# Kernel tuning notes

Measured on AMD Instinct MI355X. Metric: run time of the kernel, lower is better.

## Reference

```python
import jax, jax.numpy as jnp
import numpy as np

N_NODES = 50000
N_EDGES = 1000000
IN_CH = 256
HID_CH = 128
HEADS = 2
OUT_CH = 3
NEG_SLOPE = 0.2  # PyG GATConv default leaky_relu slope


def setup_inputs() -> dict:
    key = jax.random.key(0)
    ks = jax.random.split(key, 10)
    s = 0.1
    x = jax.random.normal(ks[0], (N_NODES, IN_CH), dtype=jnp.float32)
    edge_index = jax.random.randint(ks[1], (2, N_EDGES), 0, N_NODES, dtype=jnp.int64)
    # GATConv layer 1 (heads=2, concat=True)
    W1 = jax.random.normal(ks[2], (IN_CH, HEADS * HID_CH), dtype=jnp.float32) * s
    a_src1 = jax.random.normal(ks[3], (HEADS, HID_CH), dtype=jnp.float32) * s
    a_dst1 = jax.random.normal(ks[4], (HEADS, HID_CH), dtype=jnp.float32) * s
    b1 = jnp.zeros((HEADS * HID_CH,), dtype=jnp.float32)
    # GATConv layer 2 (heads=1, concat=False)
    W2 = jax.random.normal(ks[5], (HEADS * HID_CH, OUT_CH), dtype=jnp.float32) * s
    a_src2 = jax.random.normal(ks[6], (1, OUT_CH), dtype=jnp.float32) * s
    a_dst2 = jax.random.normal(ks[7], (1, OUT_CH), dtype=jnp.float32) * s
    b2 = jnp.zeros((OUT_CH,), dtype=jnp.float32)
    return dict(x=x, edge_index=edge_index, W1=W1, a_src1=a_src1, a_dst1=a_dst1,
                b1=b1, W2=W2, a_src2=a_src2, a_dst2=a_dst2, b2=b2)


def gat_layer(x, edge_index, W, a_src, a_dst, b, concat):
    # x: [N, F_in]; W: [F_in, H*C]; a_src/a_dst: [H, C]
    n = x.shape[0]
    H, C = a_src.shape
    h = (x @ W).reshape(n, H, C)                       # [N, H, C]
    al_s = jnp.einsum('nhc,hc->nh', h, a_src)          # [N, H]
    al_d = jnp.einsum('nhc,hc->nh', h, a_dst)          # [N, H]
    src, dst = edge_index[0], edge_index[1]
    e = jax.nn.leaky_relu(al_s[src] + al_d[dst], NEG_SLOPE)   # [E, H]
    # segment softmax over incoming edges of each dst node
    e_max = jax.ops.segment_max(e, dst, num_segments=n)       # [N, H]
    w = jnp.exp(e - e_max[dst])                                # [E, H]
    denom = jax.ops.segment_sum(w, dst, num_segments=n)        # [N, H]
    alpha = w / jnp.maximum(denom[dst], 1e-16)                 # [E, H]
    out = jax.ops.segment_sum(h[src] * alpha[:, :, None], dst, num_segments=n)  # [N, H, C]
    out = out.reshape(n, H * C) if concat else out.mean(axis=1)
    return out + b


def reference(x, edge_index, W1, a_src1, a_dst1, b1, W2, a_src2, a_dst2, b2):
    # dropout(p=0.6) is identity in eval mode
    h = jax.nn.elu(gat_layer(x, edge_index, W1, a_src1, a_dst1, b1, concat=True))
    h = gat_layer(h, edge_index, W2, a_src2, a_dst2, b2, concat=False)
    return jax.nn.log_softmax(h, axis=1)
```

## Files before the change

kernel.cpp:

```cpp
#include <hip/hip_runtime.h>

#define N_NODES 50000
#define N_EDGES 1000000
#define FIN 256
#define F1  256
#define OUTC 3
#define BUCKET 64
#define GEMM_BLOCKS ((N_NODES + 63) / 64)
#define EDGE_BLOCKS ((N_EDGES + 255) / 256)

typedef __attribute__((ext_vector_type(8))) short  short8;
typedef __attribute__((ext_vector_type(4))) float  f32x4;
typedef __attribute__((ext_vector_type(2))) float  f32x2;

__device__ __forceinline__ unsigned short f2bf(float f) {
  unsigned int x; __builtin_memcpy(&x, &f, 4);
  x += 0x7fffu + ((x >> 16) & 1u);
  return (unsigned short)(x >> 16);
}
__device__ __forceinline__ float u2f(unsigned int x) {
  float f; __builtin_memcpy(&f, &x, 4); return f;
}
__device__ __forceinline__ float wredmax(float v) {
  #pragma unroll
  for (int m = 32; m > 0; m >>= 1) v = fmaxf(v, __shfl_xor(v, m));
  return v;
}
__device__ __forceinline__ float wredsum(float v) {
  #pragma unroll
  for (int m = 32; m > 0; m >>= 1) v += __shfl_xor(v, m);
  return v;
}

__global__ __launch_bounds__(256) void k_t(const float* __restrict__ w1,
                                           unsigned short* __restrict__ w1t,
                                           int* __restrict__ deg) {
  int idx = blockIdx.x * 256 + threadIdx.x;
  int k = idx >> 8, n = idx & 255;
  w1t[n * 256 + k] = f2bf(w1[k * 256 + n]);
  if (idx < N_NODES) deg[idx] = 0;
}

__global__ __launch_bounds__(256) void k_bg(
    const float* __restrict__ x,
    const unsigned short* __restrict__ w1t,
    const float* __restrict__ a_src1,
    const float* __restrict__ a_dst1,
    unsigned short* __restrict__ h1b,
    float* __restrict__ als1,
    float* __restrict__ ald1,
    const int* __restrict__ ei,
    int* __restrict__ deg, unsigned short* __restrict__ bucket) {
  const int t = threadIdx.x;

  if (blockIdx.x >= GEMM_BLOCKS) {
    __shared__ int sflag;
    if (t < 64) {
      int idx = 2 * (t * 15625 + 7) + 1;
      unsigned long long b = __ballot(ei[idx] != 0);
      if (t == 0) sflag = (b != 0ull) ? 1 : 0;
    }
    __syncthreads();
    const int f = sflag;
    int e = (blockIdx.x - GEMM_BLOCKS) * 256 + t;
    if (e < N_EDGES) {
      int s, d;
      if (f) { s = ei[e];     d = ei[N_EDGES + e]; }
      else   { s = ei[2 * e]; d = ei[2 * (N_EDGES + e)]; }
      int pos = atomicAdd(&deg[d], 1);
      if (pos < BUCKET) bucket[d * BUCKET + pos] = (unsigned short)s;
    }
    return;
  }

  const int wv   = t >> 6;
  const int lane = t & 63;
  const int m    = lane & 15;
  const int quad = lane >> 4;
  const int row0 = blockIdx.x * 64 + wv * 16;

  int arow = row0 + m;
  if (arow > N_NODES - 1) arow = N_NODES - 1;
  const float* xrow = x + (size_t)arow * FIN + quad * 8;

  short8 af[8];
  #pragma unroll
  for (int kk = 0; kk < 8; ++kk) {
    f32x4 v0 = *(const f32x4*)(xrow + kk * 32);
    f32x4 v1 = *(const f32x4*)(xrow + kk * 32 + 4);
    short8 fr;
    #pragma unroll
    for (int j = 0; j < 4; ++j) {
      fr[j]     = (short)f2bf(v0[j]);
      fr[j + 4] = (short)f2bf(v1[j]);
    }
    af[kk] = fr;
  }

  f32x4 acc[16];
  #pragma unroll
  for (int c = 0; c < 16; ++c) {
    const unsigned short* bp = w1t + (size_t)(c * 16 + m) * FIN + quad * 8;
    f32x4 a = {0.f, 0.f, 0.f, 0.f};
    #pragma unroll
    for (int kk = 0; kk < 8; ++kk) {
      short8 bf = *(const short8*)(bp + kk * 32);
      a = __builtin_amdgcn_mfma_f32_16x16x32_bf16(af[kk], bf, a, 0, 0, 0);
    }
    acc[c] = a;
  }

  float s0[4] = {0,0,0,0}, s1[4] = {0,0,0,0}, d0[4] = {0,0,0,0}, d1[4] = {0,0,0,0};
  #pragma unroll
  for (int c = 0; c < 16; ++c) {
    int ch = c * 16 + m;
    float av = a_src1[ch];
    float dv = a_dst1[ch];
    if (c < 8) {
      #pragma unroll
      for (int r = 0; r < 4; ++r) { s0[r] += acc[c][r] * av; d0[r] += acc[c][r] * dv; }
    } else {
      #pragma unroll
      for (int r = 0; r < 4; ++r) { s1[r] += acc[c][r] * av; d1[r] += acc[c][r] * dv; }
    }
  }
  #pragma unroll
  for (int msk = 1; msk < 16; msk <<= 1) {
    #pragma unroll
    for (int r = 0; r < 4; ++r) {
      s0[r] += __shfl_xor(s0[r], msk);
      s1[r] += __shfl_xor(s1[r], msk);
      d0[r] += __shfl_xor(d0[r], msk);
      d1[r] += __shfl_xor(d1[r], msk);
    }
  }
  #pragma unroll
  for (int r = 0; r < 4; ++r) {
    int row = row0 + quad * 4 + r;
    if (row < N_NODES) {
      unsigned short* hrow = h1b + (size_t)row * F1 + m;
      #pragma unroll
      for (int c = 0; c < 16; ++c) hrow[c * 16] = f2bf(acc[c][r]);
      if (m == 0) {
        als1[row * 2 + 0] = s0[r]; als1[row * 2 + 1] = s1[r];
        ald1[row * 2 + 0] = d0[r]; ald1[row * 2 + 1] = d1[r];
      }
    }
  }
}

__global__ __launch_bounds__(256) void k_attn1(
    const unsigned short* __restrict__ bucket,
    const int* __restrict__ deg,
    const float* __restrict__ als1,
    const float* __restrict__ ald1,
    const unsigned short* __restrict__ h1b,
    const float* __restrict__ b1,
    const float* __restrict__ w2,
    const float* __restrict__ a_src2,
    const float* __restrict__ a_dst2,
    float4* __restrict__ h2pack,
    float* __restrict__ ald2) {
  const int wv   = threadIdx.x >> 6;
  const int lane = threadIdx.x & 63;
  const int n = blockIdx.x * 4 + wv;
  if (n >= N_NODES) return;
  const int dg = min(deg[n], BUCKET);
  const float ad0  = ald1[n * 2 + 0];
  const float ad1v = ald1[n * 2 + 1];
  const float2* alsv = (const float2*)als1;

  const int l31   = lane & 31;
  const int ehalf = lane >> 5;
  const bool head1 = (l31 >= 16);

  float l0 = -1e30f, l1 = -1e30f; int sreg = 0;
  if (lane < dg) {
    sreg = (int)bucket[n * BUCKET + lane];
    float2 a = alsv[sreg];
    l0 = a.x + ad0;  l0 = l0 > 0.f ? l0 : 0.2f * l0;
    l1 = a.y + ad1v; l1 = l1 > 0.f ? l1 : 0.2f * l1;
  }
  const float m0 = wredmax(l0), m1 = wredmax(l1);
  const float e0 = (lane < dg) ? __expf(l0 - m0) : 0.f;
  const float e1 = (lane < dg) ? __expf(l1 - m1) : 0.f;
  const float sum0 = wredsum(e0), sum1 = wredsum(e1);
  const float inv = 1.f / fmaxf(head1 ? sum1 : sum0, 1e-16f);

  f32x2 accv[4] = {{0.f,0.f},{0.f,0.f},{0.f,0.f},{0.f,0.f}};
  const int pairs = (dg + 1) >> 1;
  for (int e = 0; e < pairs; e += 4) {
    float w[4]; int sv[4];
    #pragma unroll
    for (int k = 0; k < 4; ++k) {
      int eidx = 2 * (e + k) + ehalf;
      int esel = eidx & 63;
      float w0 = __shfl(e0, esel);
      float w1 = __shfl(e1, esel);
      sv[k] = __shfl(sreg, esel);
      w[k] = head1 ? w1 : w0;
      if (eidx >= dg) w[k] = 0.f;
    }
    uint4 hv[4];
    #pragma unroll
    for (int k = 0; k < 4; ++k)
      hv[k] = *(const uint4*)(h1b + (size_t)sv[k] * F1 + l31 * 8);
    #pragma unroll
    for (int k = 0; k < 4; ++k) {
      const unsigned int* hu = (const unsigned int*)&hv[k];
      f32x2 wv2 = {w[k], w[k]};
      #pragma unroll
      for (int j = 0; j < 4; ++j) {
        unsigned int u = hu[j];
        f32x2 h;
        h.x = u2f(u << 16);
        h.y = u2f(u & 0xffff0000u);
        accv[j] = __builtin_elementwise_fma(wv2, h, accv[j]);
      }
    }
  }

  float* av = (float*)accv;
  #pragma unroll
  for (int j = 0; j < 8; ++j) av[j] += __shfl_xor(av[j], 32);

  float p0 = 0.f, p1 = 0.f, p2 = 0.f;
  #pragma unroll
  for (int j = 0; j < 8; ++j) {
    int ch = l31 * 8 + j;
    float tt = av[j] * inv + b1[ch];
    tt = tt > 0.f ? tt : __expf(tt) - 1.f;
    p0 = fmaf(tt, w2[ch * 3 + 0], p0);
    p1 = fmaf(tt, w2[ch * 3 + 1], p1);
    p2 = fmaf(tt, w2[ch * 3 + 2], p2);
  }
  p0 = wredsum(p0) * 0.5f;
  p1 = wredsum(p1) * 0.5f;
  p2 = wredsum(p2) * 0.5f;
  if (lane == 0) {
    float als2v = p0 * a_src2[0] + p1 * a_src2[1] + p2 * a_src2[2];
    h2pack[n] = make_float4(p0, p1, p2, als2v);
    ald2[n] = p0 * a_dst2[0] + p1 * a_dst2[1] + p2 * a_dst2[2];
  }
}

__global__ __launch_bounds__(256) void k_attn2(
    const unsigned short* __restrict__ bucket,
    const int* __restrict__ deg,
    const float4* __restrict__ h2pack,
    const float* __restrict__ ald2,
    const float* __restrict__ b2,
    float* __restrict__ out) {
  const int wv   = threadIdx.x >> 6;
  const int lane = threadIdx.x & 63;
  const int n = blockIdx.x * 4 + wv;
  if (n >= N_NODES) return;
  const int dg = min(deg[n], BUCKET);
  const float adn = ald2[n];

  float l = -1e30f;
  float4 hp = make_float4(0.f, 0.f, 0.f, 0.f);
  if (lane < dg) {
    int s = (int)bucket[n * BUCKET + lane];
    hp = h2pack[s];
    l = hp.w + adn;
    l = l > 0.f ? l : 0.2f * l;
  }
  const float m = wredmax(l);
  const float e = (lane < dg) ? __expf(l - m) : 0.f;
  const float sum = wredsum(e);
  const float inv = 1.f / fmaxf(sum, 1e-16f);
  float p0 = wredsum(e * hp.x);
  float p1 = wredsum(e * hp.y);
  float p2 = wredsum(e * hp.z);

  if (lane == 0) {
    float o0 = p0 * inv + b2[0];
    float o1 = p1 * inv + b2[1];
    float o2 = p2 * inv + b2[2];
    float mm = fmaxf(o0, fmaxf(o1, o2));
    float ls = logf(__expf(o0 - mm) + __expf(o1 - mm) + __expf(o2 - mm));
    out[n * 3 + 0] = o0 - mm - ls;
    out[n * 3 + 1] = o1 - mm - ls;
    out[n * 3 + 2] = o2 - mm - ls;
  }
}

extern "C" void kernel_launch(void* const* d_in, const int* in_sizes, int n_in,
                              void* d_out, int out_size, void* d_ws, size_t ws_size,
                              hipStream_t stream) {
  (void)in_sizes; (void)n_in; (void)out_size; (void)ws_size;
  const float* x      = (const float*)d_in[0];
  const int*   ei     = (const int*)d_in[1];
  const float* W1     = (const float*)d_in[2];
  const float* a_src1 = (const float*)d_in[3];
  const float* a_dst1 = (const float*)d_in[4];
  const float* b1     = (const float*)d_in[5];
  const float* W2     = (const float*)d_in[6];
  const float* a_src2 = (const float*)d_in[7];
  const float* a_dst2 = (const float*)d_in[8];
  const float* b2     = (const float*)d_in[9];
  float* out = (float*)d_out;

  char* p = (char*)d_ws;
  auto alloc = [&](size_t bytes) -> char* {
    char* r = p; p += (bytes + 511) & ~(size_t)511; return r;
  };
  unsigned short* w1t  = (unsigned short*)alloc(65536ull * 2);
  unsigned short* h1b  = (unsigned short*)alloc((size_t)N_NODES * F1 * 2);
  float*  als1   = (float*)alloc((size_t)N_NODES * 2 * 4);
  float*  ald1   = (float*)alloc((size_t)N_NODES * 2 * 4);
  float4* h2pack = (float4*)alloc((size_t)N_NODES * 16);
  float*  ald2   = (float*)alloc((size_t)N_NODES * 4);
  int*    deg    = (int*)alloc((size_t)N_NODES * 4);
  unsigned short* bucket = (unsigned short*)alloc((size_t)N_NODES * BUCKET * 2);

  hipLaunchKernelGGL(k_t, dim3(256), dim3(256), 0, stream, W1, w1t, deg);
  hipLaunchKernelGGL(k_bg, dim3(GEMM_BLOCKS + EDGE_BLOCKS), dim3(256), 0, stream,
                     x, w1t, a_src1, a_dst1, h1b, als1, ald1, ei, deg, bucket);
  hipLaunchKernelGGL(k_attn1, dim3((N_NODES + 3) / 4), dim3(256), 0, stream,
                     bucket, deg, als1, ald1, h1b, b1, W2, a_src2, a_dst2,
                     h2pack, ald2);
  hipLaunchKernelGGL(k_attn2, dim3((N_NODES + 3) / 4), dim3(256), 0, stream,
                     bucket, deg, h2pack, ald2, b2, out);
}
```

Baseline: 250.7 us.

## Split GEMM output columns across waves, 16 rows per block

The fused GEMM block now handles 16 rows, and each of its four waves computes a quarter of the 256 output columns, where before each wave computed all columns for its own 16 rows. This cuts per-wave accumulator registers and raises block count, which should improve occupancy and latency hiding. In exchange, every wave loads the same x rows (four times the x reads per block), and the attention-logit dot products now need a shared-memory reduction and a barrier. Bounds checks were dropped because 50000 divides evenly by 16.

```diff
diff --git a/kernel.cpp b/kernel.cpp
--- a/kernel.cpp
+++ b/kernel.cpp
@@ -6,7 +6,7 @@
 #define F1  256
 #define OUTC 3
 #define BUCKET 64
-#define GEMM_BLOCKS ((N_NODES + 63) / 64)
+#define GEMM_BLOCKS (N_NODES / 16)
 #define EDGE_BLOCKS ((N_EDGES + 255) / 256)
 
 typedef __attribute__((ext_vector_type(8))) short  short8;
@@ -77,12 +77,9 @@
   const int lane = t & 63;
   const int m    = lane & 15;
   const int quad = lane >> 4;
-  const int row0 = blockIdx.x * 64 + wv * 16;
-
-  int arow = row0 + m;
-  if (arow > N_NODES - 1) arow = N_NODES - 1;
-  const float* xrow = x + (size_t)arow * FIN + quad * 8;
-
+  const int row0 = blockIdx.x * 16;
+
+  const float* xrow = x + (size_t)(row0 + m) * FIN + quad * 8;
   short8 af[8];
   #pragma unroll
   for (int kk = 0; kk < 8; ++kk) {
@@ -97,9 +94,10 @@
     af[kk] = fr;
   }
 
-  f32x4 acc[16];
-  #pragma unroll
-  for (int c = 0; c < 16; ++c) {
+  f32x4 acc[4];
+  #pragma unroll
+  for (int cc = 0; cc < 4; ++cc) {
+    const int c = wv * 4 + cc;
     const unsigned short* bp = w1t + (size_t)(c * 16 + m) * FIN + quad * 8;
     f32x4 a = {0.f, 0.f, 0.f, 0.f};
     #pragma unroll
@@ -107,45 +105,52 @@
       short8 bf = *(const short8*)(bp + kk * 32);
       a = __builtin_amdgcn_mfma_f32_16x16x32_bf16(af[kk], bf, a, 0, 0, 0);
     }
-    acc[c] = a;
-  }
-
-  float s0[4] = {0,0,0,0}, s1[4] = {0,0,0,0}, d0[4] = {0,0,0,0}, d1[4] = {0,0,0,0};
-  #pragma unroll
-  for (int c = 0; c < 16; ++c) {
-    int ch = c * 16 + m;
+    acc[cc] = a;
+  }
+
+  float s[4] = {0,0,0,0}, d[4] = {0,0,0,0};
+  #pragma unroll
+  for (int cc = 0; cc < 4; ++cc) {
+    int ch = (wv * 4 + cc) * 16 + m;
     float av = a_src1[ch];
     float dv = a_dst1[ch];
-    if (c < 8) {
-      #pragma unroll
-      for (int r = 0; r < 4; ++r) { s0[r] += acc[c][r] * av; d0[r] += acc[c][r] * dv; }
-    } else {
-      #pragma unroll
-      for (int r = 0; r < 4; ++r) { s1[r] += acc[c][r] * av; d1[r] += acc[c][r] * dv; }
-    }
+    #pragma unroll
+    for (int r = 0; r < 4; ++r) { s[r] += acc[cc][r] * av; d[r] += acc[cc][r] * dv; }
   }
   #pragma unroll
   for (int msk = 1; msk < 16; msk <<= 1) {
     #pragma unroll
     for (int r = 0; r < 4; ++r) {
-      s0[r] += __shfl_xor(s0[r], msk);
-      s1[r] += __shfl_xor(s1[r], msk);
-      d0[r] += __shfl_xor(d0[r], msk);
-      d1[r] += __shfl_xor(d1[r], msk);
-    }
-  }
+      s[r] += __shfl_xor(s[r], msk);
+      d[r] += __shfl_xor(d[r], msk);
+    }
+  }
+
+  __shared__ float reds[4][16];
+  __shared__ float redd[4][16];
+  if (m == 0) {
+    #pragma unroll
+    for (int r = 0; r < 4; ++r) {
+      reds[wv][quad * 4 + r] = s[r];
+      redd[wv][quad * 4 + r] = d[r];
+    }
+  }
+
   #pragma unroll
   for (int r = 0; r < 4; ++r) {
     int row = row0 + quad * 4 + r;
-    if (row < N_NODES) {
-      unsigned short* hrow = h1b + (size_t)row * F1 + m;
-      #pragma unroll
-      for (int c = 0; c < 16; ++c) hrow[c * 16] = f2bf(acc[c][r]);
-      if (m == 0) {
-        als1[row * 2 + 0] = s0[r]; als1[row * 2 + 1] = s1[r];
-        ald1[row * 2 + 0] = d0[r]; ald1[row * 2 + 1] = d1[r];
-      }
-    }
+    unsigned short* hrow = h1b + (size_t)row * F1 + m;
+    #pragma unroll
+    for (int cc = 0; cc < 4; ++cc) hrow[(wv * 4 + cc) * 16] = f2bf(acc[cc][r]);
+  }
+
+  __syncthreads();
+  if (t < 16) {
+    int row = row0 + t;
+    als1[row * 2 + 0] = reds[0][t] + reds[1][t];
+    als1[row * 2 + 1] = reds[2][t] + reds[3][t];
+    ald1[row * 2 + 0] = redd[0][t] + redd[1][t];
+    ald1[row * 2 + 1] = redd[2][t] + redd[3][t];
   }
 }
 
```

After: 328.4 us. 1.31x slower.

## Split layer-1 attention into alpha, column-chunked aggregation, and post kernels

Applied to the files above, without the earlier changes.

The fused layer-1 attention kernel is split into three kernels. The first computes normalized softmax weights per edge slot and writes them to global memory. The second aggregates neighbor features in 8 column chunks of 32 channels each, launched as separate blocks so that each chunk's gathered slice of h1b can stay in cache. The third applies bias, ELU and the W2 projection from an fp16 intermediate. In exchange it adds two extra launches and roughly 25MB of extra alpha writes, plus a 25MB fp16 round-trip with some precision loss.

```diff
diff --git a/kernel.cpp b/kernel.cpp
--- a/kernel.cpp
+++ b/kernel.cpp
@@ -8,10 +8,14 @@
 #define BUCKET 64
 #define GEMM_BLOCKS ((N_NODES + 63) / 64)
 #define EDGE_BLOCKS ((N_EDGES + 255) / 256)
+#define NODE_BLOCKS ((N_NODES + 3) / 4)
+#define NCHUNK 8
 
 typedef __attribute__((ext_vector_type(8))) short  short8;
 typedef __attribute__((ext_vector_type(4))) float  f32x4;
 typedef __attribute__((ext_vector_type(2))) float  f32x2;
+typedef __attribute__((ext_vector_type(8))) _Float16 h16x8;
+typedef __attribute__((ext_vector_type(4))) _Float16 h16x4;
 
 __device__ __forceinline__ unsigned short f2bf(float f) {
   unsigned int x; __builtin_memcpy(&x, &f, 4);
@@ -149,12 +153,93 @@
   }
 }
 
-__global__ __launch_bounds__(256) void k_attn1(
+__global__ __launch_bounds__(256) void k_alpha(
     const unsigned short* __restrict__ bucket,
     const int* __restrict__ deg,
     const float* __restrict__ als1,
     const float* __restrict__ ald1,
+    float* __restrict__ alpha0,
+    float* __restrict__ alpha1) {
+  const int wv   = threadIdx.x >> 6;
+  const int lane = threadIdx.x & 63;
+  const int n = blockIdx.x * 4 + wv;
+  if (n >= N_NODES) return;
+  const int dg = min(deg[n], BUCKET);
+  const float ad0  = ald1[n * 2 + 0];
+  const float ad1v = ald1[n * 2 + 1];
+  const float2* alsv = (const float2*)als1;
+
+  float l0 = -1e30f, l1 = -1e30f;
+  if (lane < dg) {
+    int s = (int)bucket[n * BUCKET + lane];
+    float2 a = alsv[s];
+    l0 = a.x + ad0;  l0 = l0 > 0.f ? l0 : 0.2f * l0;
+    l1 = a.y + ad1v; l1 = l1 > 0.f ? l1 : 0.2f * l1;
+  }
+  const float m0 = wredmax(l0), m1 = wredmax(l1);
+  const float e0 = (lane < dg) ? __expf(l0 - m0) : 0.f;
+  const float e1 = (lane < dg) ? __expf(l1 - m1) : 0.f;
+  const float sum0 = wredsum(e0), sum1 = wredsum(e1);
+  alpha0[n * BUCKET + lane] = e0 / fmaxf(sum0, 1e-16f);
+  alpha1[n * BUCKET + lane] = e1 / fmaxf(sum1, 1e-16f);
+}
+
+__global__ __launch_bounds__(256) void k_agg(
+    const unsigned short* __restrict__ bucket,
+    const int* __restrict__ deg,
+    const float* __restrict__ alpha0,
+    const float* __restrict__ alpha1,
     const unsigned short* __restrict__ h1b,
+    _Float16* __restrict__ h2agg) {
+  const int chunk = blockIdx.x / NODE_BLOCKS;
+  const int nb    = blockIdx.x % NODE_BLOCKS;
+  const int wv   = threadIdx.x >> 6;
+  const int lane = threadIdx.x & 63;
+  const int n = nb * 4 + wv;
+  if (n >= N_NODES) return;
+  const int dg = min(deg[n], BUCKET);
+  const int eg = lane >> 2;
+  const int cl = lane & 3;
+  const int ch0 = chunk * 32 + cl * 8;
+
+  const float* aarr = (chunk >= 4) ? alpha1 : alpha0;
+  const float areg = aarr[n * BUCKET + lane];
+  const int   sreg = (lane < dg) ? (int)bucket[n * BUCKET + lane] : 0;
+
+  f32x2 acc[4] = {{0.f,0.f},{0.f,0.f},{0.f,0.f},{0.f,0.f}};
+  for (int g = 0; g < dg; g += 16) {
+    int slot = g + eg;
+    float a = __shfl(areg, slot);
+    int   s = __shfl(sreg, slot);
+    uint4 hv = *(const uint4*)(h1b + (size_t)s * F1 + ch0);
+    const unsigned int* hu = (const unsigned int*)&hv;
+    f32x2 wv2 = {a, a};
+    #pragma unroll
+    for (int j = 0; j < 4; ++j) {
+      unsigned int u = hu[j];
+      f32x2 h;
+      h.x = u2f(u << 16);
+      h.y = u2f(u & 0xffff0000u);
+      acc[j] = __builtin_elementwise_fma(wv2, h, acc[j]);
+    }
+  }
+
+  float* av = (float*)acc;
+  #pragma unroll
+  for (int msk = 4; msk < 64; msk <<= 1) {
+    #pragma unroll
+    for (int j = 0; j < 8; ++j) av[j] += __shfl_xor(av[j], msk);
+  }
+  if (eg == 0) {
+    h16x8 o;
+    #pragma unroll
+    for (int j = 0; j < 8; ++j) o[j] = (_Float16)av[j];
+    *(h16x8*)(h2agg + (size_t)n * F1 + ch0) = o;
+  }
+}
+
+__global__ __launch_bounds__(256) void k_post(
+    const _Float16* __restrict__ h2agg,
     const float* __restrict__ b1,
     const float* __restrict__ w2,
     const float* __restrict__ a_src2,
@@ -165,78 +250,20 @@
   const int lane = threadIdx.x & 63;
   const int n = blockIdx.x * 4 + wv;
   if (n >= N_NODES) return;
-  const int dg = min(deg[n], BUCKET);
-  const float ad0  = ald1[n * 2 + 0];
-  const float ad1v = ald1[n * 2 + 1];
-  const float2* alsv = (const float2*)als1;
-
-  const int l31   = lane & 31;
-  const int ehalf = lane >> 5;
-  const bool head1 = (l31 >= 16);
-
-  float l0 = -1e30f, l1 = -1e30f; int sreg = 0;
-  if (lane < dg) {
-    sreg = (int)bucket[n * BUCKET + lane];
-    float2 a = alsv[sreg];
-    l0 = a.x + ad0;  l0 = l0 > 0.f ? l0 : 0.2f * l0;
-    l1 = a.y + ad1v; l1 = l1 > 0.f ? l1 : 0.2f * l1;
-  }
-  const float m0 = wredmax(l0), m1 = wredmax(l1);
-  const float e0 = (lane < dg) ? __expf(l0 - m0) : 0.f;
-  const float e1 = (lane < dg) ? __expf(l1 - m1) : 0.f;
-  const float sum0 = wredsum(e0), sum1 = wredsum(e1);
-  const float inv = 1.f / fmaxf(head1 ? sum1 : sum0, 1e-16f);
-
-  f32x2 accv[4] = {{0.f,0.f},{0.f,0.f},{0.f,0.f},{0.f,0.f}};
-  const int pairs = (dg + 1) >> 1;
-  for (int e = 0; e < pairs; e += 4) {
-    float w[4]; int sv[4];
-    #pragma unroll
-    for (int k = 0; k < 4; ++k) {
-      int eidx = 2 * (e + k) + ehalf;
-      int esel = eidx & 63;
-      float w0 = __shfl(e0, esel);
-      float w1 = __shfl(e1, esel);
-      sv[k] = __shfl(sreg, esel);
-      w[k] = head1 ? w1 : w0;
-      if (eidx >= dg) w[k] = 0.f;
-    }
-    uint4 hv[4];
-    #pragma unroll
-    for (int k = 0; k < 4; ++k)
-      hv[k] = *(const uint4*)(h1b + (size_t)sv[k] * F1 + l31 * 8);
-    #pragma unroll
-    for (int k = 0; k < 4; ++k) {
-      const unsigned int* hu = (const unsigned int*)&hv[k];
-      f32x2 wv2 = {w[k], w[k]};
-      #pragma unroll
-      for (int j = 0; j < 4; ++j) {
-        unsigned int u = hu[j];
-        f32x2 h;
-        h.x = u2f(u << 16);
-        h.y = u2f(u & 0xffff0000u);
-        accv[j] = __builtin_elementwise_fma(wv2, h, accv[j]);
-      }
-    }
-  }
-
-  float* av = (float*)accv;
-  #pragma unroll
-  for (int j = 0; j < 8; ++j) av[j] += __shfl_xor(av[j], 32);
-
+  h16x4 hv = *(const h16x4*)(h2agg + (size_t)n * F1 + lane * 4);
   float p0 = 0.f, p1 = 0.f, p2 = 0.f;
   #pragma unroll
-  for (int j = 0; j < 8; ++j) {
-    int ch = l31 * 8 + j;
-    float tt = av[j] * inv + b1[ch];
+  for (int j = 0; j < 4; ++j) {
+    int ch = lane * 4 + j;
+    float tt = (float)hv[j] + b1[ch];
     tt = tt > 0.f ? tt : __expf(tt) - 1.f;
     p0 = fmaf(tt, w2[ch * 3 + 0], p0);
     p1 = fmaf(tt, w2[ch * 3 + 1], p1);
     p2 = fmaf(tt, w2[ch * 3 + 2], p2);
   }
-  p0 = wredsum(p0) * 0.5f;
-  p1 = wredsum(p1) * 0.5f;
-  p2 = wredsum(p2) * 0.5f;
+  p0 = wredsum(p0);
+  p1 = wredsum(p1);
+  p2 = wredsum(p2);
   if (lane == 0) {
     float als2v = p0 * a_src2[0] + p1 * a_src2[1] + p2 * a_src2[2];
     h2pack[n] = make_float4(p0, p1, p2, als2v);
@@ -314,13 +341,19 @@
   float*  ald2   = (float*)alloc((size_t)N_NODES * 4);
   int*    deg    = (int*)alloc((size_t)N_NODES * 4);
   unsigned short* bucket = (unsigned short*)alloc((size_t)N_NODES * BUCKET * 2);
+  float*  alpha0 = (float*)alloc((size_t)N_NODES * BUCKET * 4);
+  float*  alpha1 = (float*)alloc((size_t)N_NODES * BUCKET * 4);
+  _Float16* h2agg = (_Float16*)alloc((size_t)N_NODES * F1 * 2);
 
   hipLaunchKernelGGL(k_t, dim3(256), dim3(256), 0, stream, W1, w1t, deg);
   hipLaunchKernelGGL(k_bg, dim3(GEMM_BLOCKS + EDGE_BLOCKS), dim3(256), 0, stream,
                      x, w1t, a_src1, a_dst1, h1b, als1, ald1, ei, deg, bucket);
-  hipLaunchKernelGGL(k_attn1, dim3((N_NODES + 3) / 4), dim3(256), 0, stream,
-                     bucket, deg, als1, ald1, h1b, b1, W2, a_src2, a_dst2,
-                     h2pack, ald2);
-  hipLaunchKernelGGL(k_attn2, dim3((N_NODES + 3) / 4), dim3(256), 0, stream,
+  hipLaunchKernelGGL(k_alpha, dim3(NODE_BLOCKS), dim3(256), 0, stream,
+                     bucket, deg, als1, ald1, alpha0, alpha1);
+  hipLaunchKernelGGL(k_agg, dim3(NCHUNK * NODE_BLOCKS), dim3(256), 0, stream,
+                     bucket, deg, alpha0, alpha1, h1b, h2agg);
+  hipLaunchKernelGGL(k_post, dim3(NODE_BLOCKS), dim3(256), 0, stream,
+                     h2agg, b1, W2, a_src2, a_dst2, h2pack, ald2);
+  hipLaunchKernelGGL(k_attn2, dim3(NODE_BLOCKS), dim3(256), 0, stream,
                      bucket, deg, h2pack, ald2, b2, out);
 }
```

Result: slower. 362.9 us (+44.7%).

## Fold W1 transpose into GEMM kernel with atomic flag spin-wait

Applied to the files above, without the earlier changes.

Removes the separate transpose/zeroing kernel and runs the W1 transpose as the first 256 blocks of the fused GEMM/bucketing kernel. GEMM blocks spin on a global atomic counter until all transpose blocks are done, and a memset zeroes the degree array and flag. This trades one kernel launch boundary for an intra-kernel dependency, which relies on transpose blocks being scheduled before GEMM blocks and risks deadlock or stalls if they are not.

```diff
diff --git a/kernel.cpp b/kernel.cpp
--- a/kernel.cpp
+++ b/kernel.cpp
@@ -6,6 +6,7 @@
 #define F1  256
 #define OUTC 3
 #define BUCKET 64
+#define TP_BLOCKS 256
 #define GEMM_BLOCKS ((N_NODES + 63) / 64)
 #define EDGE_BLOCKS ((N_EDGES + 255) / 256)
 
@@ -32,28 +33,34 @@
   return v;
 }
 
-__global__ __launch_bounds__(256) void k_t(const float* __restrict__ w1,
-                                           unsigned short* __restrict__ w1t,
-                                           int* __restrict__ deg) {
-  int idx = blockIdx.x * 256 + threadIdx.x;
-  int k = idx >> 8, n = idx & 255;
-  w1t[n * 256 + k] = f2bf(w1[k * 256 + n]);
-  if (idx < N_NODES) deg[idx] = 0;
-}
-
 __global__ __launch_bounds__(256) void k_bg(
+    const float* __restrict__ w1,
     const float* __restrict__ x,
-    const unsigned short* __restrict__ w1t,
+    unsigned short* __restrict__ w1t,
     const float* __restrict__ a_src1,
     const float* __restrict__ a_dst1,
     unsigned short* __restrict__ h1b,
     float* __restrict__ als1,
     float* __restrict__ ald1,
     const int* __restrict__ ei,
-    int* __restrict__ deg, unsigned short* __restrict__ bucket) {
+    int* __restrict__ deg,
+    unsigned short* __restrict__ bucket) {
   const int t = threadIdx.x;
-
-  if (blockIdx.x >= GEMM_BLOCKS) {
+  int* flag = deg + N_NODES;
+
+  if (blockIdx.x < TP_BLOCKS) {
+    int idx = blockIdx.x * 256 + t;
+    int k = idx >> 8, n = idx & 255;
+    w1t[n * 256 + k] = f2bf(w1[k * 256 + n]);
+    __syncthreads();
+    if (t == 0) {
+      __threadfence();
+      atomicAdd(flag, 1);
+    }
+    return;
+  }
+
+  if (blockIdx.x >= TP_BLOCKS + GEMM_BLOCKS) {
     __shared__ int sflag;
     if (t < 64) {
       int idx = 2 * (t * 15625 + 7) + 1;
@@ -62,7 +69,7 @@
     }
     __syncthreads();
     const int f = sflag;
-    int e = (blockIdx.x - GEMM_BLOCKS) * 256 + t;
+    int e = (blockIdx.x - TP_BLOCKS - GEMM_BLOCKS) * 256 + t;
     if (e < N_EDGES) {
       int s, d;
       if (f) { s = ei[e];     d = ei[N_EDGES + e]; }
@@ -73,11 +80,18 @@
     return;
   }
 
+  if (t == 0) {
+    while (__hip_atomic_load(flag, __ATOMIC_RELAXED, __HIP_MEMORY_SCOPE_AGENT) < TP_BLOCKS)
+      __builtin_amdgcn_s_sleep(8);
+  }
+  __syncthreads();
+  (void)__hip_atomic_load(flag, __ATOMIC_ACQUIRE, __HIP_MEMORY_SCOPE_AGENT);
+
   const int wv   = t >> 6;
   const int lane = t & 63;
   const int m    = lane & 15;
   const int quad = lane >> 4;
-  const int row0 = blockIdx.x * 64 + wv * 16;
+  const int row0 = (blockIdx.x - TP_BLOCKS) * 64 + wv * 16;
 
   int arow = row0 + m;
   if (arow > N_NODES - 1) arow = N_NODES - 1;
@@ -312,12 +326,12 @@
   float*  ald1   = (float*)alloc((size_t)N_NODES * 2 * 4);
   float4* h2pack = (float4*)alloc((size_t)N_NODES * 16);
   float*  ald2   = (float*)alloc((size_t)N_NODES * 4);
-  int*    deg    = (int*)alloc((size_t)N_NODES * 4);
+  int*    deg    = (int*)alloc(((size_t)N_NODES + 1) * 4);
   unsigned short* bucket = (unsigned short*)alloc((size_t)N_NODES * BUCKET * 2);
 
-  hipLaunchKernelGGL(k_t, dim3(256), dim3(256), 0, stream, W1, w1t, deg);
-  hipLaunchKernelGGL(k_bg, dim3(GEMM_BLOCKS + EDGE_BLOCKS), dim3(256), 0, stream,
-                     x, w1t, a_src1, a_dst1, h1b, als1, ald1, ei, deg, bucket);
+  hipMemsetAsync(deg, 0, ((size_t)N_NODES + 1) * 4, stream);
+  hipLaunchKernelGGL(k_bg, dim3(TP_BLOCKS + GEMM_BLOCKS + EDGE_BLOCKS), dim3(256), 0, stream,
+                     W1, x, w1t, a_src1, a_dst1, h1b, als1, ald1, ei, deg, bucket);
   hipLaunchKernelGGL(k_attn1, dim3((N_NODES + 3) / 4), dim3(256), 0, stream,
                      bucket, deg, als1, ald1, h1b, b1, W2, a_src2, a_dst2,
                      h2pack, ald2);
```

Measured after the change: 305.1 us. 1.22x slower.
